# Kernel optimization log

Hardware: AMD Instinct MI355X
Metric: run time of the kernel (lower is better)

## Reference

```python
import jax, jax.numpy as jnp
import numpy as np
from jax import lax

B, C, H, W = 2, 64, 48, 64
RU, RV = 3, 3
U, V = 2 * RU + 1, 2 * RV + 1
D = U * V  # 49 displacements


def setup_inputs() -> dict:
    key = jax.random.key(0)
    ks = jax.random.split(key, 12)
    p = lambda k, shape, s: jax.random.normal(k, shape, jnp.float32) * s
    feat1 = p(ks[0], (B, C, H, W), 1.0)
    feat2 = p(ks[1], (B, C, H, W), 1.0)
    gy, gx = jnp.meshgrid(jnp.arange(H, dtype=jnp.float32), jnp.arange(W, dtype=jnp.float32), indexing='ij')
    base = jnp.broadcast_to(jnp.stack([gx, gy])[None], (B, 2, H, W))  # channel0=x, channel1=y
    coords = base + p(ks[2], (B, 2, H, W), 1.5)
    return {
        'feat1': feat1, 'feat2': feat2, 'coords': coords,
        # MatchingNet (ConvBlock = conv+ReLU, BN folded into conv)
        'w0': p(ks[3], (96, 2 * C, 3, 3), 0.06), 'b0': jnp.zeros((96,), jnp.float32),
        'w1': p(ks[4], (128, 96, 3, 3), 0.05), 'b1': jnp.zeros((128,), jnp.float32),
        'w2': p(ks[5], (128, 128, 3, 3), 0.04), 'b2': jnp.zeros((128,), jnp.float32),
        'w3': p(ks[6], (64, 128, 3, 3), 0.04), 'b3': jnp.zeros((64,), jnp.float32),
        'wd': p(ks[7], (32, 64, 4, 4), 0.05), 'bd': jnp.zeros((32,), jnp.float32),  # deconv k4 s2 p1
        'w5': p(ks[8], (1, 32, 3, 3), 0.1), 'b5': jnp.zeros((1,), jnp.float32),
        # Displacement-aware projection: 1x1 conv over the 49 displacement channels
        'wdap': p(ks[9], (D, D), 0.15),
    }


def _conv(x, w, b, stride=1, pad=1):
    y = lax.conv_general_dilated(x, w, (stride, stride), ((pad, pad), (pad, pad)),
                                 dimension_numbers=('NCHW', 'OIHW', 'NCHW'))
    return y + b[None, :, None, None]


def _warp_with_context(feat2, coords):
    # grid_sample(bilinear, zeros padding, align_corners=True) at coords + every displacement
    b, c, h, w = feat2.shape
    du = jnp.arange(-RU, RU + 1, dtype=feat2.dtype)
    dv = jnp.arange(-RV, RV + 1, dtype=feat2.dtype)
    x = coords[:, 0][:, None, None, :, :] + du[None, None, :, None, None]  # (b,V,U,h,w) via broadcast
    y = coords[:, 1][:, None, None, :, :] + dv[None, :, None, None, None]
    x0 = jnp.floor(x); y0 = jnp.floor(y)
    wx = (x - x0)[:, None]; wy = (y - y0)[:, None]  # (b,1,V,U,h,w)
    x0i = x0.astype(jnp.int32); y0i = y0.astype(jnp.int32)
    feat_flat = feat2.reshape(b, c, h * w)

    def gather(xi, yi):
        valid = (xi >= 0) & (xi < w) & (yi >= 0) & (yi < h)
        idx = jnp.clip(yi, 0, h - 1) * w + jnp.clip(xi, 0, w - 1)
        v = jax.vmap(lambda f, i: f[:, i])(feat_flat, idx.reshape(b, -1))  # (b,c,P)
        v = v.reshape(b, c, V, U, h, w)
        return v * valid[:, None].astype(feat2.dtype)

    v00 = gather(x0i, y0i)
    v01 = gather(x0i + 1, y0i)
    v10 = gather(x0i, y0i + 1)
    v11 = gather(x0i + 1, y0i + 1)
    out = v00 * (1 - wx) * (1 - wy) + v01 * wx * (1 - wy) + v10 * (1 - wx) * wy + v11 * wx * wy
    return out.transpose(0, 2, 3, 1, 4, 5)  # (b, V, U, c, h, w)


def reference(feat1, feat2, coords, w0, b0, w1, b1, w2, b2, w3, b3, wd, bd, w5, b5, wdap):
    b, c, h, w = feat1.shape
    f2 = _warp_with_context(feat2, coords)
    f1 = jnp.broadcast_to(feat1[:, None, None], (b, V, U, c, h, w))
    feat = jnp.concatenate([f1, f2], axis=3).reshape(b * V * U, 2 * c, h, w)
    # MatchingNet
    x = jnp.maximum(_conv(feat, w0, b0), 0)
    x = jnp.maximum(_conv(x, w1, b1, stride=2), 0)
    x = jnp.maximum(_conv(x, w2, b2), 0)
    x = jnp.maximum(_conv(x, w3, b3), 0)
    x = lax.conv_general_dilated(x, wd, (1, 1), ((2, 2), (2, 2)), lhs_dilation=(2, 2),
                                 dimension_numbers=('NCHW', 'OIHW', 'NCHW')) + bd[None, :, None, None]
    x = jnp.maximum(x, 0)
    cost = _conv(x, w5, b5).reshape(b, V, U, h, w)
    # DAP: 1x1 conv across the D displacement channels, no bias
    cost = jnp.einsum('ed,bdhw->behw', wdap, cost.reshape(b, D, h, w)).reshape(b, V, U, h, w)
    prob = jax.nn.softmax(cost.reshape(b, D, h, w), axis=1).reshape(b, V, U, h, w)
    du = jnp.arange(-RU, RU + 1, dtype=feat1.dtype)
    dv = jnp.arange(-RV, RV + 1, dtype=feat1.dtype)
    dx = jnp.sum(prob * du[None, None, :, None, None], axis=(1, 2))
    dy = jnp.sum(prob * dv[None, :, None, None, None], axis=(1, 2))
    return coords + jnp.stack([dx, dy], axis=1)
```

## Files before the change

kernel.cpp:

```cpp
#include <hip/hip_runtime.h>
#include <hip/hip_bf16.h>

using bf16 = __hip_bfloat16;
typedef __attribute__((ext_vector_type(8))) __bf16 bf16x8;
typedef __attribute__((ext_vector_type(4))) float f32x4;

static __device__ __forceinline__ bf16 f2b(float v) { return __float2bfloat16(v); }
static __device__ __forceinline__ float us2f(unsigned short u) {
    return __uint_as_float(((unsigned)u) << 16);
}


__global__ void sentinel_k(float* __restrict__ out, int nel, float val) {
    int i = blockIdx.x * 256 + threadIdx.x;
    if (i < nel) out[i] = val;
}

__global__ void pack_all(const float* __restrict__ w0, const float* __restrict__ w1,
                         const float* __restrict__ w2, const float* __restrict__ w3,
                         const float* __restrict__ wd, bf16* __restrict__ wsw0,
                         bf16* __restrict__ wsw0a, bf16* __restrict__ wsw1,
                         bf16* __restrict__ wsw2, bf16* __restrict__ wsw3,
                         bf16* __restrict__ wswd) {
    int i = blockIdx.x * 256 + threadIdx.x;
    if (i < 110592) {
        int icbase = (i < 55296) ? 64 : 0;
        bf16* dst = (i < 55296) ? wsw0 : wsw0a;
        int o = (i < 55296) ? i : i - 55296;
        int j = o & 7, lane = (o >> 3) & 63;
        int m = lane & 15, q = lane >> 4;
        int cc = (o >> 9) & 1;
        int fragid = o >> 10;
        int t = fragid / 6, ocf = fragid % 6;
        int oc = ocf * 16 + m, ic = cc * 32 + q * 8 + j;
        dst[o] = f2b(w0[((size_t)oc * 128 + icbase + ic) * 9 + t]);
    } else if (i < 307200) {
        int o = i - 110592;
        int j = o & 7, lane = (o >> 3) & 63;
        int m = lane & 15, q = lane >> 4;
        int cc = (o >> 9) % 12;
        int fragid = (o >> 9) / 12;
        int t2 = fragid / 8, ocf = fragid % 8;
        int oc = ocf * 16 + m;
        int pc = cc * 32 + q * 8 + j;
        int dy = (t2 < 2) ? -1 : 0;
        int dx = (t2 & 1) ? 0 : -1;
        int p = pc / 96, ic = pc % 96;
        int py = p >> 1, px = p & 1;
        int ky = (dy == -1) ? (py == 1 ? 0 : -1) : (py == 0 ? 1 : 2);
        int kx = (dx == -1) ? (px == 1 ? 0 : -1) : (px == 0 ? 1 : 2);
        float v = (ky >= 0 && kx >= 0) ? w1[((size_t)oc * 96 + ic) * 9 + ky * 3 + kx] : 0.f;
        wsw1[o] = f2b(v);
    } else if (i < 454656) {
        int o = i - 307200;
        int j = o & 7, lane = (o >> 3) & 63;
        int m = lane & 15, q = lane >> 4;
        int cc = (o >> 9) % 4;
        int fragid = (o >> 9) / 4;
        int t = fragid / 8, ocf = fragid % 8;
        int oc = ocf * 16 + m, ic = cc * 32 + q * 8 + j;
        wsw2[o] = f2b(w2[((size_t)oc * 128 + ic) * 9 + t]);
    } else if (i < 528384) {
        int o = i - 454656;
        int j = o & 7, lane = (o >> 3) & 63;
        int m = lane & 15, q = lane >> 4;
        int cc = (o >> 9) % 4;
        int fragid = (o >> 9) / 4;
        int t = fragid / 4, ocf = fragid % 4;
        int oc = ocf * 16 + m, ic = cc * 32 + q * 8 + j;
        wsw3[o] = f2b(w3[((size_t)oc * 128 + ic) * 9 + t]);
    } else if (i < 561152) {
        int o = i - 528384;
        int j = o & 7, lane = (o >> 3) & 63;
        int m = lane & 15, q = lane >> 4;
        int cc = (o >> 9) & 1;
        int ocf = (o >> 10) & 1;
        int t2 = (o >> 11) & 3;
        int c = o >> 13;
        int oc = ocf * 16 + m, ic = cc * 32 + q * 8 + j;
        int qy = c >> 1, qx = c & 1;
        int dy = qy - 1 + (t2 >> 1), dx = qx - 1 + (t2 & 1);
        int ky = (qy == 0) ? (dy == -1 ? 0 : 2) : (dy == 0 ? 1 : 3);
        int kx = (qx == 0) ? (dx == -1 ? 0 : 2) : (dx == 0 ? 1 : 3);
        wswd[o] = f2b(wd[((size_t)oc * 64 + ic) * 16 + ky * 4 + kx]);
    }
}

__global__ void to_nhwc2(const float* __restrict__ feat1, const float* __restrict__ feat2,
                         bf16* __restrict__ f1n, bf16* __restrict__ f2n) {
    int i = blockIdx.x * 256 + threadIdx.x;
    const float* src = (i < 393216) ? feat1 : feat2;
    bf16* dst = (i < 393216) ? f1n : f2n;
    int o = (i < 393216) ? i : i - 393216;
    if (o >= 393216) return;
    int c = o & 63;
    int p = (o >> 6) % 3072;
    int b = o / (3072 * 64);
    dst[o] = f2b(src[((size_t)b * 64 + c) * 3072 + p]);
}

__global__ __launch_bounds__(256) void warp_kernel(const bf16* __restrict__ f2n,
                                                   const float* __restrict__ coords,
                                                   bf16* __restrict__ f2w, int bd0, int cnt) {
    int idx = blockIdx.x * 256 + threadIdx.x;
    if (idx >= cnt * 3072 * 8) return;
    int g = idx & 7;
    int pix = idx >> 3;
    int p = pix % 3072;
    int z = pix / 3072;
    int bd = bd0 + z;
    int b = bd / 49, d = bd % 49;
    float du = (float)(d % 7 - 3), dv = (float)(d / 7 - 3);
    float cx = coords[(size_t)(b * 2 + 0) * 3072 + p] + du;
    float cy = coords[(size_t)(b * 2 + 1) * 3072 + p] + dv;
    float x0f = floorf(cx), y0f = floorf(cy);
    float wx = cx - x0f, wy = cy - y0f;
    int x0 = (int)x0f, y0 = (int)y0f;
    int x1 = x0 + 1, y1 = y0 + 1;
    bool vx0 = (x0 >= 0) && (x0 < 64), vx1 = (x1 >= 0) && (x1 < 64);
    bool vy0 = (y0 >= 0) && (y0 < 48), vy1 = (y1 >= 0) && (y1 < 48);
    int xc0 = min(max(x0, 0), 63), xc1 = min(max(x1, 0), 63);
    int yc0 = min(max(y0, 0), 47), yc1 = min(max(y1, 0), 47);
    float w00 = (vx0 && vy0) ? (1.f - wx) * (1.f - wy) : 0.f;
    float w01 = (vx1 && vy0) ? wx * (1.f - wy) : 0.f;
    float w10 = (vx0 && vy1) ? (1.f - wx) * wy : 0.f;
    float w11 = (vx1 && vy1) ? wx * wy : 0.f;
    const unsigned short* f2 = (const unsigned short*)f2n + (size_t)b * 3072 * 64 + g * 8;
    ushort4 a0 = *(const ushort4*)(f2 + (size_t)(yc0 * 64 + xc0) * 64);
    ushort4 a1 = *(const ushort4*)(f2 + (size_t)(yc0 * 64 + xc0) * 64 + 4);
    ushort4 b0v = *(const ushort4*)(f2 + (size_t)(yc0 * 64 + xc1) * 64);
    ushort4 b1v = *(const ushort4*)(f2 + (size_t)(yc0 * 64 + xc1) * 64 + 4);
    ushort4 c0 = *(const ushort4*)(f2 + (size_t)(yc1 * 64 + xc0) * 64);
    ushort4 c1 = *(const ushort4*)(f2 + (size_t)(yc1 * 64 + xc0) * 64 + 4);
    ushort4 d0 = *(const ushort4*)(f2 + (size_t)(yc1 * 64 + xc1) * 64);
    ushort4 d1 = *(const ushort4*)(f2 + (size_t)(yc1 * 64 + xc1) * 64 + 4);
    unsigned short ua[8] = {a0.x, a0.y, a0.z, a0.w, a1.x, a1.y, a1.z, a1.w};
    unsigned short ub[8] = {b0v.x, b0v.y, b0v.z, b0v.w, b1v.x, b1v.y, b1v.z, b1v.w};
    unsigned short uc[8] = {c0.x, c0.y, c0.z, c0.w, c1.x, c1.y, c1.z, c1.w};
    unsigned short ud[8] = {d0.x, d0.y, d0.z, d0.w, d1.x, d1.y, d1.z, d1.w};
    unsigned short ro[8];
#pragma unroll
    for (int e = 0; e < 8; ++e) {
        float v = w00 * us2f(ua[e]) + w01 * us2f(ub[e]) + w10 * us2f(uc[e]) + w11 * us2f(ud[e]);
        bf16 r = f2b(v);
        ro[e] = *(unsigned short*)&r;
    }
    unsigned short* outp = (unsigned short*)f2w + ((size_t)z * 3072 + p) * 64 + g * 8;
    *(ushort4*)outp = (ushort4){ro[0], ro[1], ro[2], ro[3]};
    *(ushort4*)(outp + 4) = (ushort4){ro[4], ro[5], ro[6], ro[7]};
}

template <int IC, int OCTOT, int OC_BLK, int H, int W, int MROWS, int NTAPS, int DXW,
          int DYLO, int DXLO, int BMODE, int OMODE>
__global__ __launch_bounds__(512, 4) void conv_ldz(const bf16* __restrict__ in_,
                                                   const bf16* __restrict__ wsw_,
                                                   const float* __restrict__ bias,
                                                   const bf16* __restrict__ base_,
                                                   bf16* __restrict__ out, int bd0, int cnt) {
    constexpr int NCH = IC / 32;
    constexpr int NfT = OC_BLK / 32;
    constexpr int TPXH = MROWS * W / 2;
    constexpr int MF = TPXH / 16;
    constexpr int NDY = NTAPS / DXW;
    constexpr int ROWS_IN = MROWS + NDY - 1;
    constexpr int COLS_IN = W + DXW - 1;
    constexpr int NOCF = OCTOT / 16;
    constexpr int PITCH = 40;
    constexpr int SZA = ROWS_IN * COLS_IN * PITCH;
    constexpr int OUTSH = MROWS * W * OC_BLK;
    constexpr int SMEM = (2 * SZA > OUTSH) ? 2 * SZA : OUTSH;
    __shared__ __align__(16) unsigned short s_mem[SMEM];

    const unsigned short* in = (const unsigned short*)in_;
    const unsigned short* wsw = (const unsigned short*)wsw_;
    const unsigned short* baseh = (const unsigned short*)base_;
    const int tid = threadIdx.x;
    const int wave = tid >> 6, lane = tid & 63;
    const int m = lane & 15, q = lane >> 4;
    const int wz = wave >> 2, wy = (wave >> 1) & 1, wx = wave & 1;
    const int bx = blockIdx.x, by = blockIdx.y;
    const int z0 = blockIdx.z * 2;
    const int zw = z0 + wz;
    const bool zok = zw < cnt;
    const int foff = m * PITCH + q * 8;
    const int ocbase = by * OC_BLK;

    f32x4 acc[MF][NfT];
#pragma unroll
    for (int a = 0; a < MF; ++a)
#pragma unroll
        for (int nf = 0; nf < NfT; ++nf) acc[a][nf] = (f32x4){0.f, 0.f, 0.f, 0.f};

    for (int cc = 0; cc < NCH; ++cc) {
        constexpr int SZE = ROWS_IN * COLS_IN * 4;
        for (int i = tid; i < 2 * SZE; i += 512) {
            int zz = i / SZE;
            int r2 = i % SZE;
            int e = r2 & 3;
            int pix = r2 >> 2;
            int cI = pix % COLS_IN;
            int rr = pix / COLS_IN;
            int gy = bx * MROWS + rr + DYLO;
            int gx = cI + DXLO;
            uint4 v = {0u, 0u, 0u, 0u};
            if ((z0 + zz) < cnt && gy >= 0 && gy < H && gx >= 0 && gx < W)
                v = *(const uint4*)(in +
                                    ((size_t)((z0 + zz) * H + gy) * W + gx) * IC + cc * 32 + e * 8);
            *(uint4*)(&s_mem[zz * SZA + pix * PITCH + e * 8]) = v;
        }
        __syncthreads();
        if (zok) {
            bf16x8 bcur[NfT], bnxt[NfT];
#pragma unroll
            for (int nf = 0; nf < NfT; ++nf) {
                const int fragoc = (ocbase >> 4) + wx * NfT + nf;
                bcur[nf] = *(const bf16x8*)(wsw + (((size_t)0 * NOCF + fragoc) * NCH + cc) * 512 +
                                            lane * 8);
            }
#pragma unroll
            for (int t = 0; t < NTAPS; ++t) {
                if (t + 1 < NTAPS) {
#pragma unroll
                    for (int nf = 0; nf < NfT; ++nf) {
                        const int fragoc = (ocbase >> 4) + wx * NfT + nf;
                        bnxt[nf] = *(const bf16x8*)(wsw +
                                                    (((size_t)(t + 1) * NOCF + fragoc) * NCH + cc) *
                                                        512 +
                                                    lane * 8);
                    }
                }
                bf16x8 af[MF];
#pragma unroll
                for (int mf = 0; mf < MF; ++mf) {
                    const int pxb = wy * TPXH + mf * 16;
                    const int yl = pxb / W, xb = pxb % W;
                    const unsigned short* pa =
                        &s_mem[wz * SZA + ((yl + t / DXW) * COLS_IN + xb + t % DXW) * PITCH] + foff;
                    af[mf] = *(const bf16x8*)pa;
                }
#pragma unroll
                for (int mf = 0; mf < MF; ++mf)
#pragma unroll
                    for (int nf = 0; nf < NfT; ++nf)
                        acc[mf][nf] = __builtin_amdgcn_mfma_f32_16x16x32_bf16(af[mf], bcur[nf],
                                                                              acc[mf][nf], 0, 0, 0);
                if (t + 1 < NTAPS) {
#pragma unroll
                    for (int nf = 0; nf < NfT; ++nf) bcur[nf] = bnxt[nf];
                }
            }
        }
        __syncthreads();
    }

    const int bimg = (bd0 + zw) / 49;
    float bb[NfT];
    if constexpr (BMODE == 0) {
#pragma unroll
        for (int nf = 0; nf < NfT; ++nf) bb[nf] = bias[ocbase + wx * (OC_BLK / 2) + nf * 16 + m];
    }
    for (int zz = 0; zz < 2; ++zz) {
        if (wz == zz && zok) {
#pragma unroll
            for (int mf = 0; mf < MF; ++mf) {
                const int pxb = wy * TPXH + mf * 16;
#pragma unroll
                for (int r = 0; r < 4; ++r) {
                    const int px = pxb + q * 4 + r;
                    const int yl = px / W, xl = px % W;
                    const int gy = bx * MROWS + yl;
#pragma unroll
                    for (int nf = 0; nf < NfT; ++nf) {
                        const int oc = wx * (OC_BLK / 2) + nf * 16 + m;
                        float v = acc[mf][nf][r];
                        if constexpr (BMODE == 1)
                            v += us2f(baseh[(((size_t)bimg * 48 + gy) * 64 + xl) * 96 + ocbase + oc]);
                        else
                            v += bb[nf];
                        if constexpr (OMODE != 4) v = fmaxf(v, 0.f);
                        bf16 bv = f2b(v);
                        s_mem[px * OC_BLK + oc] = *(unsigned short*)&bv;
                    }
                }
            }
        }
        __syncthreads();
        const int z = z0 + zz;
        if (z < cnt) {
            constexpr int TOT16 = MROWS * W * OC_BLK / 8;
            for (int g = tid; g < TOT16; g += 512) {
                const int o = g * 8;
                if constexpr (OMODE == 1) {
                    const int xx = o / 384;
                    const int rr = o % 384;
                    const int pp = rr / 96;
                    const int oco = rr % 96;
                    const int px = (pp >> 1) * 64 + 2 * xx + (pp & 1);
                    uint4 vv = *(const uint4*)&s_mem[px * 96 + oco];
                    *(uint4*)((unsigned short*)out + (((size_t)z * 24 + bx) * 32 + xx) * 384 + rr) =
                        vv;
                } else {
                    uint4 vv = *(const uint4*)&s_mem[o];
                    const int px = o / OC_BLK;
                    const int oco = o % OC_BLK;
                    const int gy = bx * MROWS + px / W;
                    const int xl = px % W;
                    if constexpr (OMODE == 4)
                        *(uint4*)((unsigned short*)out +
                                  (((size_t)z * H + gy) * W + xl) * OCTOT + ocbase + oco) = vv;
                    else
                        *(uint4*)((unsigned short*)out +
                                  (((size_t)z * H + gy) * W + xl) * OCTOT + ocbase + oco) = vv;
                }
            }
        }
        __syncthreads();
    }
}

__global__ __launch_bounds__(512, 4) void deconv_k4(const bf16* __restrict__ in_,
                                                    const bf16* __restrict__ wswd_,
                                                    const float* __restrict__ bias,
                                                    bf16* __restrict__ out, int cnt) {
    constexpr int PITCH = 40;
    constexpr int SZA = 6 * 34 * PITCH;
    __shared__ __align__(16) unsigned short s_mem[16384];

    const unsigned short* in = (const unsigned short*)in_;
    const unsigned short* wsw = (const unsigned short*)wswd_;
    const int tid = threadIdx.x;
    const int wave = tid >> 6, lane = tid & 63;
    const int m = lane & 15, q = lane >> 4;
    const int wz = wave >> 2, cls = wave & 3;
    const int qy = cls >> 1, qx = cls & 1;
    const int bx = blockIdx.x;
    const int z0 = blockIdx.z * 2;
    const int zw = z0 + wz;
    const bool zok = zw < cnt;
    const int foff = m * PITCH + q * 8;

    f32x4 acc[8][2];
#pragma unroll
    for (int a = 0; a < 8; ++a) {
        acc[a][0] = (f32x4){0.f, 0.f, 0.f, 0.f};
        acc[a][1] = (f32x4){0.f, 0.f, 0.f, 0.f};
    }

    for (int cc = 0; cc < 2; ++cc) {
        constexpr int SZE = 6 * 34 * 4;
        for (int i = tid; i < 2 * SZE; i += 512) {
            int zz = i / SZE;
            int r2 = i % SZE;
            int e = r2 & 3;
            int pix = r2 >> 2;
            int cI = pix % 34;
            int rr = pix / 34;
            int gy = bx * 4 + rr - 1;
            int gx = cI - 1;
            uint4 v = {0u, 0u, 0u, 0u};
            if ((z0 + zz) < cnt && gy >= 0 && gy < 24 && gx >= 0 && gx < 32)
                v = *(const uint4*)(in + ((size_t)((z0 + zz) * 24 + gy) * 32 + gx) * 64 + cc * 32 +
                                    e * 8);
            *(uint4*)(&s_mem[zz * SZA + pix * PITCH + e * 8]) = v;
        }
        __syncthreads();
        if (zok) {
            bf16x8 bcur[2], bnxt[2];
#pragma unroll
            for (int nf = 0; nf < 2; ++nf)
                bcur[nf] = *(const bf16x8*)(wsw + cls * 8192 + 0 * 2048 + nf * 1024 + cc * 512 +
                                            lane * 8);
#pragma unroll
            for (int t = 0; t < 4; ++t) {
                if (t + 1 < 4) {
#pragma unroll
                    for (int nf = 0; nf < 2; ++nf)
                        bnxt[nf] = *(const bf16x8*)(wsw + cls * 8192 + (t + 1) * 2048 + nf * 1024 +
                                                    cc * 512 + lane * 8);
                }
                const int dy = qy - 1 + (t >> 1);
                const int dx = qx - 1 + (t & 1);
                bf16x8 af[8];
#pragma unroll
                for (int mf = 0; mf < 8; ++mf) {
                    const int yl = mf >> 1, xb = (mf & 1) * 16;
                    const unsigned short* pa =
                        &s_mem[wz * SZA + ((yl + dy + 1) * 34 + xb + dx + 1) * PITCH] + foff;
                    af[mf] = *(const bf16x8*)pa;
                }
#pragma unroll
                for (int mf = 0; mf < 8; ++mf)
#pragma unroll
                    for (int nf = 0; nf < 2; ++nf)
                        acc[mf][nf] = __builtin_amdgcn_mfma_f32_16x16x32_bf16(af[mf], bcur[nf],
                                                                              acc[mf][nf], 0, 0, 0);
                if (t + 1 < 4) {
                    bcur[0] = bnxt[0];
                    bcur[1] = bnxt[1];
                }
            }
        }
        __syncthreads();
    }

    const float bb0 = bias[m], bb1 = bias[16 + m];
    for (int zz = 0; zz < 2; ++zz) {
        if (wz == zz && zok) {
#pragma unroll
            for (int mf = 0; mf < 8; ++mf) {
#pragma unroll
                for (int r = 0; r < 4; ++r) {
                    const int px = mf * 16 + q * 4 + r;
                    const int yl = px >> 5, xl = px & 31;
                    const int opx = (2 * yl + qy) * 64 + 2 * xl + qx;
                    float v0 = fmaxf(acc[mf][0][r] + bb0, 0.f);
                    float v1 = fmaxf(acc[mf][1][r] + bb1, 0.f);
                    bf16 b0 = f2b(v0), b1 = f2b(v1);
                    s_mem[opx * 32 + m] = *(unsigned short*)&b0;
                    s_mem[opx * 32 + 16 + m] = *(unsigned short*)&b1;
                }
            }
        }
        __syncthreads();
        const int z = z0 + zz;
        if (z < cnt) {
            for (int g = tid; g < 2048; g += 512) {
                const int o = g * 8;
                *(uint4*)((unsigned short*)out + ((size_t)z * 3072 + bx * 512) * 32 + o) =
                    *(const uint4*)&s_mem[o];
            }
        }
        __syncthreads();
    }
}

__global__ __launch_bounds__(256) void conv5_k(const bf16* __restrict__ in_,
                                               const float* __restrict__ w5,
                                               const float* __restrict__ b5,
                                               float* __restrict__ cost, int bd0, int cnt) {
    __shared__ float s_w5[9][32];
    const int tid = threadIdx.x;
    for (int i = tid; i < 288; i += 256) {
        int ic = i % 32, t = i / 32;
        s_w5[t][ic] = w5[ic * 9 + t];
    }
    __syncthreads();
    int idx = blockIdx.x * 256 + tid;
    if (idx >= cnt * 3072) return;
    int p = idx % 3072, z = idx / 3072;
    int y = p >> 6, x = p & 63;
    const unsigned short* in = (const unsigned short*)in_;
    float acc = b5[0];
#pragma unroll
    for (int ky = 0; ky < 3; ++ky) {
        int gy = y + ky - 1;
        if (gy < 0 || gy >= 48) continue;
#pragma unroll
        for (int kx = 0; kx < 3; ++kx) {
            int gx = x + kx - 1;
            if (gx < 0 || gx >= 64) continue;
            const ushort4* src = (const ushort4*)(in + ((size_t)(z * 48 + gy) * 64 + gx) * 32);
            const float* wr = s_w5[ky * 3 + kx];
#pragma unroll
            for (int e = 0; e < 8; ++e) {
                ushort4 u = src[e];
                acc = fmaf(us2f(u.x), wr[e * 4 + 0], acc);
                acc = fmaf(us2f(u.y), wr[e * 4 + 1], acc);
                acc = fmaf(us2f(u.z), wr[e * 4 + 2], acc);
                acc = fmaf(us2f(u.w), wr[e * 4 + 3], acc);
            }
        }
    }
    cost[(size_t)(bd0 + z) * 3072 + p] = acc;
}

__global__ __launch_bounds__(256) void dap_flow(const float* __restrict__ cost,
                                                const float* __restrict__ wdap,
                                                const float* __restrict__ coords,
                                                float* __restrict__ outp) {
    __shared__ float s_w[49 * 49];
    int tid = threadIdx.x;
    for (int i = tid; i < 2401; i += 256) s_w[i] = wdap[i];
    __syncthreads();
    int idx = blockIdx.x * 256 + tid;
    if (idx >= 2 * 3072) return;
    int p = idx % 3072, b = idx / 3072;
    float c[49];
#pragma unroll
    for (int d = 0; d < 49; ++d) c[d] = cost[((size_t)(b * 49 + d)) * 3072 + p];
    float mx = -1e30f;
    for (int e = 0; e < 49; ++e) {
        float s = 0.f;
#pragma unroll
        for (int d = 0; d < 49; ++d) s = fmaf(s_w[e * 49 + d], c[d], s);
        mx = fmaxf(mx, s);
    }
    float sum = 0.f, sx = 0.f, sy = 0.f;
    for (int e = 0; e < 49; ++e) {
        float s = 0.f;
#pragma unroll
        for (int d = 0; d < 49; ++d) s = fmaf(s_w[e * 49 + d], c[d], s);
        float pr = __expf(s - mx);
        sum += pr;
        sx += pr * (float)(e % 7 - 3);
        sy += pr * (float)(e / 7 - 3);
    }
    float inv = 1.f / sum;
    outp[(size_t)(b * 2 + 0) * 3072 + p] = coords[(size_t)(b * 2 + 0) * 3072 + p] + sx * inv;
    outp[(size_t)(b * 2 + 1) * 3072 + p] = coords[(size_t)(b * 2 + 1) * 3072 + p] + sy * inv;
}

extern "C" void kernel_launch(void* const* d_in, const int* in_sizes, int n_in,
                              void* d_out, int out_size, void* d_ws, size_t ws_size,
                              hipStream_t stream) {
    (void)in_sizes; (void)n_in;
    const float* feat1 = (const float*)d_in[0];
    const float* feat2 = (const float*)d_in[1];
    const float* coords = (const float*)d_in[2];
    const float* w0 = (const float*)d_in[3];
    const float* b0 = (const float*)d_in[4];
    const float* w1 = (const float*)d_in[5];
    const float* b1 = (const float*)d_in[6];
    const float* w2 = (const float*)d_in[7];
    const float* b2 = (const float*)d_in[8];
    const float* w3 = (const float*)d_in[9];
    const float* b3 = (const float*)d_in[10];
    const float* wd = (const float*)d_in[11];
    const float* bdc = (const float*)d_in[12];
    const float* w5 = (const float*)d_in[13];
    const float* b5 = (const float*)d_in[14];
    const float* wdap = (const float*)d_in[15];
    float* outp = (float*)d_out;

    char* ws = (char*)d_ws;
    bf16* wsw0 = (bf16*)(ws + 0);
    bf16* wsw0a = (bf16*)(ws + 110592);
    bf16* wsw1 = (bf16*)(ws + 221184);
    bf16* wsw2 = (bf16*)(ws + 614400);
    bf16* wsw3 = (bf16*)(ws + 909312);
    bf16* wswd = (bf16*)(ws + 1056768);
    bf16* f1n = (bf16*)(ws + 1122304);
    bf16* part0 = (bf16*)(ws + 1908736);
    float* cost = (float*)(ws + 3088384);
    bf16* f2n = (bf16*)(ws + 4292608);
    const size_t fixed_end = 5079040;

    const int cand[7] = {98, 49, 25, 14, 7, 2, 1};
    int nb = 0;
    for (int i = 0; i < 7; ++i) {
        if (fixed_end + (size_t)983040 * cand[i] <= ws_size) { nb = cand[i]; break; }
    }
    if (nb == 0) {
        float val = 10000.f + (float)(ws_size >> 20);
        sentinel_k<<<dim3((out_size + 255) / 256), 256, 0, stream>>>(outp, out_size, val);
        return;
    }
    char* regA = ws + fixed_end;
    char* regB = regA + (size_t)393216 * nb;
    bf16* f2w = (bf16*)regA;
    bf16* x1 = (bf16*)regA;
    bf16* x3 = (bf16*)regA;
    bf16* x0p = (bf16*)regB;
    bf16* x2 = (bf16*)regB;
    bf16* xd = (bf16*)regB;

    pack_all<<<dim3(2192), 256, 0, stream>>>(w0, w1, w2, w3, wd, wsw0, wsw0a, wsw1, wsw2, wsw3,
                                             wswd);
    to_nhwc2<<<dim3(3072), 256, 0, stream>>>(feat1, feat2, f1n, f2n);
    conv_ldz<64, 96, 96, 48, 64, 2, 9, 3, -1, -1, 0, 4>
        <<<dim3(24, 1, 1), 512, 0, stream>>>(f1n, wsw0a, b0, nullptr, part0, 0, 2);

    for (int s = 0; s < 98; s += nb) {
        int cnt = (98 - s < nb) ? (98 - s) : nb;
        int zp = (cnt + 1) / 2;
        warp_kernel<<<dim3(cnt * 96), 256, 0, stream>>>(f2n, coords, f2w, s, cnt);
        conv_ldz<64, 96, 96, 48, 64, 2, 9, 3, -1, -1, 1, 1>
            <<<dim3(24, 1, zp), 512, 0, stream>>>(f2w, wsw0, nullptr, part0, x0p, s, cnt);
        conv_ldz<384, 128, 64, 24, 32, 4, 4, 2, -1, -1, 0, 0>
            <<<dim3(6, 2, zp), 512, 0, stream>>>(x0p, wsw1, b1, nullptr, x1, s, cnt);
        conv_ldz<128, 128, 64, 24, 32, 4, 9, 3, -1, -1, 0, 0>
            <<<dim3(6, 2, zp), 512, 0, stream>>>(x1, wsw2, b2, nullptr, x2, s, cnt);
        conv_ldz<128, 64, 32, 24, 32, 4, 9, 3, -1, -1, 0, 0>
            <<<dim3(6, 2, zp), 512, 0, stream>>>(x2, wsw3, b3, nullptr, x3, s, cnt);
        deconv_k4<<<dim3(6, 1, zp), 512, 0, stream>>>(x3, wswd, bdc, xd, cnt);
        conv5_k<<<dim3(cnt * 12), 256, 0, stream>>>(xd, w5, b5, cost, s, cnt);
    }

    dap_flow<<<dim3(24), 256, 0, stream>>>(cost, wdap, coords, outp);
}
```

Baseline: 389.8 us.

## Split conv blocks to one image per 256-thread block with 4-wave pixel split

Conv and deconv kernels previously processed two images per 512-thread block, with waves split over image, pixel half and OC half. They now process one image per 256-thread block, with the four waves splitting pixels and each wave covering all OC fragments. This halves shared memory per block and drops the cnt guards and per-image store loop. Each wave holds more accumulators, so register pressure goes up, and weight fragments are loaded per wave across the full OC block. The conv3 launch also changes from OC_BLK 32 with two OC blocks to a single OC block of 64.

```diff
diff --git a/kernel.cpp b/kernel.cpp
--- a/kernel.cpp
+++ b/kernel.cpp
@@ -152,15 +152,15 @@
 
 template <int IC, int OCTOT, int OC_BLK, int H, int W, int MROWS, int NTAPS, int DXW,
           int DYLO, int DXLO, int BMODE, int OMODE>
-__global__ __launch_bounds__(512, 4) void conv_ldz(const bf16* __restrict__ in_,
+__global__ __launch_bounds__(256, 4) void conv_px4(const bf16* __restrict__ in_,
                                                    const bf16* __restrict__ wsw_,
                                                    const float* __restrict__ bias,
                                                    const bf16* __restrict__ base_,
-                                                   bf16* __restrict__ out, int bd0, int cnt) {
+                                                   bf16* __restrict__ out, int bd0) {
     constexpr int NCH = IC / 32;
-    constexpr int NfT = OC_BLK / 32;
-    constexpr int TPXH = MROWS * W / 2;
-    constexpr int MF = TPXH / 16;
+    constexpr int NfT = OC_BLK / 16;
+    constexpr int TPXQ = MROWS * W / 4;
+    constexpr int MF = TPXQ / 16;
     constexpr int NDY = NTAPS / DXW;
     constexpr int ROWS_IN = MROWS + NDY - 1;
     constexpr int COLS_IN = W + DXW - 1;
@@ -168,20 +168,16 @@
     constexpr int PITCH = 40;
     constexpr int SZA = ROWS_IN * COLS_IN * PITCH;
     constexpr int OUTSH = MROWS * W * OC_BLK;
-    constexpr int SMEM = (2 * SZA > OUTSH) ? 2 * SZA : OUTSH;
+    constexpr int SMEM = (SZA > OUTSH) ? SZA : OUTSH;
     __shared__ __align__(16) unsigned short s_mem[SMEM];
 
     const unsigned short* in = (const unsigned short*)in_;
     const unsigned short* wsw = (const unsigned short*)wsw_;
     const unsigned short* baseh = (const unsigned short*)base_;
     const int tid = threadIdx.x;
-    const int wave = tid >> 6, lane = tid & 63;
+    const int wp = tid >> 6, lane = tid & 63;
     const int m = lane & 15, q = lane >> 4;
-    const int wz = wave >> 2, wy = (wave >> 1) & 1, wx = wave & 1;
-    const int bx = blockIdx.x, by = blockIdx.y;
-    const int z0 = blockIdx.z * 2;
-    const int zw = z0 + wz;
-    const bool zok = zw < cnt;
+    const int bx = blockIdx.x, by = blockIdx.y, z = blockIdx.z;
     const int foff = m * PITCH + q * 8;
     const int ocbase = by * OC_BLK;
 
@@ -193,27 +189,24 @@
 
     for (int cc = 0; cc < NCH; ++cc) {
         constexpr int SZE = ROWS_IN * COLS_IN * 4;
-        for (int i = tid; i < 2 * SZE; i += 512) {
-            int zz = i / SZE;
-            int r2 = i % SZE;
-            int e = r2 & 3;
-            int pix = r2 >> 2;
+        for (int i = tid; i < SZE; i += 256) {
+            int e = i & 3;
+            int pix = i >> 2;
             int cI = pix % COLS_IN;
             int rr = pix / COLS_IN;
             int gy = bx * MROWS + rr + DYLO;
             int gx = cI + DXLO;
             uint4 v = {0u, 0u, 0u, 0u};
-            if ((z0 + zz) < cnt && gy >= 0 && gy < H && gx >= 0 && gx < W)
-                v = *(const uint4*)(in +
-                                    ((size_t)((z0 + zz) * H + gy) * W + gx) * IC + cc * 32 + e * 8);
-            *(uint4*)(&s_mem[zz * SZA + pix * PITCH + e * 8]) = v;
+            if (gy >= 0 && gy < H && gx >= 0 && gx < W)
+                v = *(const uint4*)(in + ((size_t)(z * H + gy) * W + gx) * IC + cc * 32 + e * 8);
+            *(uint4*)(&s_mem[pix * PITCH + e * 8]) = v;
         }
         __syncthreads();
-        if (zok) {
+        {
             bf16x8 bcur[NfT], bnxt[NfT];
 #pragma unroll
             for (int nf = 0; nf < NfT; ++nf) {
-                const int fragoc = (ocbase >> 4) + wx * NfT + nf;
+                const int fragoc = (ocbase >> 4) + nf;
                 bcur[nf] = *(const bf16x8*)(wsw + (((size_t)0 * NOCF + fragoc) * NCH + cc) * 512 +
                                             lane * 8);
             }
@@ -222,7 +215,7 @@
                 if (t + 1 < NTAPS) {
 #pragma unroll
                     for (int nf = 0; nf < NfT; ++nf) {
-                        const int fragoc = (ocbase >> 4) + wx * NfT + nf;
+                        const int fragoc = (ocbase >> 4) + nf;
                         bnxt[nf] = *(const bf16x8*)(wsw +
                                                     (((size_t)(t + 1) * NOCF + fragoc) * NCH + cc) *
                                                         512 +
@@ -232,10 +225,10 @@
                 bf16x8 af[MF];
 #pragma unroll
                 for (int mf = 0; mf < MF; ++mf) {
-                    const int pxb = wy * TPXH + mf * 16;
+                    const int pxb = wp * TPXQ + mf * 16;
                     const int yl = pxb / W, xb = pxb % W;
                     const unsigned short* pa =
-                        &s_mem[wz * SZA + ((yl + t / DXW) * COLS_IN + xb + t % DXW) * PITCH] + foff;
+                        &s_mem[((yl + t / DXW) * COLS_IN + xb + t % DXW) * PITCH] + foff;
                     af[mf] = *(const bf16x8*)pa;
                 }
 #pragma unroll
@@ -253,90 +246,73 @@
         __syncthreads();
     }
 
-    const int bimg = (bd0 + zw) / 49;
+    const int bimg = (bd0 + z) / 49;
     float bb[NfT];
     if constexpr (BMODE == 0) {
 #pragma unroll
-        for (int nf = 0; nf < NfT; ++nf) bb[nf] = bias[ocbase + wx * (OC_BLK / 2) + nf * 16 + m];
-    }
-    for (int zz = 0; zz < 2; ++zz) {
-        if (wz == zz && zok) {
-#pragma unroll
-            for (int mf = 0; mf < MF; ++mf) {
-                const int pxb = wy * TPXH + mf * 16;
-#pragma unroll
-                for (int r = 0; r < 4; ++r) {
-                    const int px = pxb + q * 4 + r;
-                    const int yl = px / W, xl = px % W;
-                    const int gy = bx * MROWS + yl;
-#pragma unroll
-                    for (int nf = 0; nf < NfT; ++nf) {
-                        const int oc = wx * (OC_BLK / 2) + nf * 16 + m;
-                        float v = acc[mf][nf][r];
-                        if constexpr (BMODE == 1)
-                            v += us2f(baseh[(((size_t)bimg * 48 + gy) * 64 + xl) * 96 + ocbase + oc]);
-                        else
-                            v += bb[nf];
-                        if constexpr (OMODE != 4) v = fmaxf(v, 0.f);
-                        bf16 bv = f2b(v);
-                        s_mem[px * OC_BLK + oc] = *(unsigned short*)&bv;
-                    }
-                }
+        for (int nf = 0; nf < NfT; ++nf) bb[nf] = bias[ocbase + nf * 16 + m];
+    }
+#pragma unroll
+    for (int mf = 0; mf < MF; ++mf) {
+        const int pxb = wp * TPXQ + mf * 16;
+#pragma unroll
+        for (int r = 0; r < 4; ++r) {
+            const int px = pxb + q * 4 + r;
+            const int yl = px / W, xl = px % W;
+            const int gy = bx * MROWS + yl;
+#pragma unroll
+            for (int nf = 0; nf < NfT; ++nf) {
+                const int oc = nf * 16 + m;
+                float v = acc[mf][nf][r];
+                if constexpr (BMODE == 1)
+                    v += us2f(baseh[(((size_t)bimg * 48 + gy) * 64 + xl) * 96 + ocbase + oc]);
+                else
+                    v += bb[nf];
+                if constexpr (OMODE != 4) v = fmaxf(v, 0.f);
+                bf16 bv = f2b(v);
+                s_mem[px * OC_BLK + oc] = *(unsigned short*)&bv;
             }
         }
-        __syncthreads();
-        const int z = z0 + zz;
-        if (z < cnt) {
-            constexpr int TOT16 = MROWS * W * OC_BLK / 8;
-            for (int g = tid; g < TOT16; g += 512) {
-                const int o = g * 8;
-                if constexpr (OMODE == 1) {
-                    const int xx = o / 384;
-                    const int rr = o % 384;
-                    const int pp = rr / 96;
-                    const int oco = rr % 96;
-                    const int px = (pp >> 1) * 64 + 2 * xx + (pp & 1);
-                    uint4 vv = *(const uint4*)&s_mem[px * 96 + oco];
-                    *(uint4*)((unsigned short*)out + (((size_t)z * 24 + bx) * 32 + xx) * 384 + rr) =
-                        vv;
-                } else {
-                    uint4 vv = *(const uint4*)&s_mem[o];
-                    const int px = o / OC_BLK;
-                    const int oco = o % OC_BLK;
-                    const int gy = bx * MROWS + px / W;
-                    const int xl = px % W;
-                    if constexpr (OMODE == 4)
-                        *(uint4*)((unsigned short*)out +
-                                  (((size_t)z * H + gy) * W + xl) * OCTOT + ocbase + oco) = vv;
-                    else
-                        *(uint4*)((unsigned short*)out +
-                                  (((size_t)z * H + gy) * W + xl) * OCTOT + ocbase + oco) = vv;
-                }
-            }
-        }
-        __syncthreads();
-    }
-}
-
-__global__ __launch_bounds__(512, 4) void deconv_k4(const bf16* __restrict__ in_,
+    }
+    __syncthreads();
+    constexpr int TOT16 = MROWS * W * OC_BLK / 8;
+    for (int g = tid; g < TOT16; g += 256) {
+        const int o = g * 8;
+        if constexpr (OMODE == 1) {
+            const int xx = o / 384;
+            const int rr = o % 384;
+            const int pp = rr / 96;
+            const int oco = rr % 96;
+            const int px = (pp >> 1) * 64 + 2 * xx + (pp & 1);
+            uint4 vv = *(const uint4*)&s_mem[px * 96 + oco];
+            *(uint4*)((unsigned short*)out + (((size_t)z * 24 + bx) * 32 + xx) * 384 + rr) = vv;
+        } else {
+            uint4 vv = *(const uint4*)&s_mem[o];
+            const int px = o / OC_BLK;
+            const int oco = o % OC_BLK;
+            const int gy = bx * MROWS + px / W;
+            const int xl = px % W;
+            *(uint4*)((unsigned short*)out + (((size_t)z * H + gy) * W + xl) * OCTOT + ocbase +
+                      oco) = vv;
+        }
+    }
+}
+
+__global__ __launch_bounds__(256, 4) void deconv_c4(const bf16* __restrict__ in_,
                                                     const bf16* __restrict__ wswd_,
                                                     const float* __restrict__ bias,
-                                                    bf16* __restrict__ out, int cnt) {
+                                                    bf16* __restrict__ out) {
     constexpr int PITCH = 40;
-    constexpr int SZA = 6 * 34 * PITCH;
     __shared__ __align__(16) unsigned short s_mem[16384];
 
     const unsigned short* in = (const unsigned short*)in_;
     const unsigned short* wsw = (const unsigned short*)wswd_;
     const int tid = threadIdx.x;
-    const int wave = tid >> 6, lane = tid & 63;
+    const int cls = tid >> 6, lane = tid & 63;
     const int m = lane & 15, q = lane >> 4;
-    const int wz = wave >> 2, cls = wave & 3;
     const int qy = cls >> 1, qx = cls & 1;
     const int bx = blockIdx.x;
-    const int z0 = blockIdx.z * 2;
-    const int zw = z0 + wz;
-    const bool zok = zw < cnt;
+    const int z = blockIdx.y;
     const int foff = m * PITCH + q * 8;
 
     f32x4 acc[8][2];
@@ -348,28 +324,24 @@
 
     for (int cc = 0; cc < 2; ++cc) {
         constexpr int SZE = 6 * 34 * 4;
-        for (int i = tid; i < 2 * SZE; i += 512) {
-            int zz = i / SZE;
-            int r2 = i % SZE;
-            int e = r2 & 3;
-            int pix = r2 >> 2;
+        for (int i = tid; i < SZE; i += 256) {
+            int e = i & 3;
+            int pix = i >> 2;
             int cI = pix % 34;
             int rr = pix / 34;
             int gy = bx * 4 + rr - 1;
             int gx = cI - 1;
             uint4 v = {0u, 0u, 0u, 0u};
-            if ((z0 + zz) < cnt && gy >= 0 && gy < 24 && gx >= 0 && gx < 32)
-                v = *(const uint4*)(in + ((size_t)((z0 + zz) * 24 + gy) * 32 + gx) * 64 + cc * 32 +
-                                    e * 8);
-            *(uint4*)(&s_mem[zz * SZA + pix * PITCH + e * 8]) = v;
+            if (gy >= 0 && gy < 24 && gx >= 0 && gx < 32)
+                v = *(const uint4*)(in + ((size_t)(z * 24 + gy) * 32 + gx) * 64 + cc * 32 + e * 8);
+            *(uint4*)(&s_mem[pix * PITCH + e * 8]) = v;
         }
         __syncthreads();
-        if (zok) {
+        {
             bf16x8 bcur[2], bnxt[2];
 #pragma unroll
             for (int nf = 0; nf < 2; ++nf)
-                bcur[nf] = *(const bf16x8*)(wsw + cls * 8192 + 0 * 2048 + nf * 1024 + cc * 512 +
-                                            lane * 8);
+                bcur[nf] = *(const bf16x8*)(wsw + cls * 8192 + nf * 1024 + cc * 512 + lane * 8);
 #pragma unroll
             for (int t = 0; t < 4; ++t) {
                 if (t + 1 < 4) {
@@ -385,7 +357,7 @@
                 for (int mf = 0; mf < 8; ++mf) {
                     const int yl = mf >> 1, xb = (mf & 1) * 16;
                     const unsigned short* pa =
-                        &s_mem[wz * SZA + ((yl + dy + 1) * 34 + xb + dx + 1) * PITCH] + foff;
+                        &s_mem[((yl + dy + 1) * 34 + xb + dx + 1) * PITCH] + foff;
                     af[mf] = *(const bf16x8*)pa;
                 }
 #pragma unroll
@@ -404,33 +376,25 @@
     }
 
     const float bb0 = bias[m], bb1 = bias[16 + m];
-    for (int zz = 0; zz < 2; ++zz) {
-        if (wz == zz && zok) {
-#pragma unroll
-            for (int mf = 0; mf < 8; ++mf) {
-#pragma unroll
-                for (int r = 0; r < 4; ++r) {
-                    const int px = mf * 16 + q * 4 + r;
-                    const int yl = px >> 5, xl = px & 31;
-                    const int opx = (2 * yl + qy) * 64 + 2 * xl + qx;
-                    float v0 = fmaxf(acc[mf][0][r] + bb0, 0.f);
-                    float v1 = fmaxf(acc[mf][1][r] + bb1, 0.f);
-                    bf16 b0 = f2b(v0), b1 = f2b(v1);
-                    s_mem[opx * 32 + m] = *(unsigned short*)&b0;
-                    s_mem[opx * 32 + 16 + m] = *(unsigned short*)&b1;
-                }
-            }
-        }
-        __syncthreads();
-        const int z = z0 + zz;
-        if (z < cnt) {
-            for (int g = tid; g < 2048; g += 512) {
-                const int o = g * 8;
-                *(uint4*)((unsigned short*)out + ((size_t)z * 3072 + bx * 512) * 32 + o) =
-                    *(const uint4*)&s_mem[o];
-            }
-        }
-        __syncthreads();
+#pragma unroll
+    for (int mf = 0; mf < 8; ++mf) {
+#pragma unroll
+        for (int r = 0; r < 4; ++r) {
+            const int px = mf * 16 + q * 4 + r;
+            const int yl = px >> 5, xl = px & 31;
+            const int opx = (2 * yl + qy) * 64 + 2 * xl + qx;
+            float v0 = fmaxf(acc[mf][0][r] + bb0, 0.f);
+            float v1 = fmaxf(acc[mf][1][r] + bb1, 0.f);
+            bf16 b0 = f2b(v0), b1 = f2b(v1);
+            s_mem[opx * 32 + m] = *(unsigned short*)&b0;
+            s_mem[opx * 32 + 16 + m] = *(unsigned short*)&b1;
+        }
+    }
+    __syncthreads();
+    for (int g = tid; g < 2048; g += 256) {
+        const int o = g * 8;
+        *(uint4*)((unsigned short*)out + ((size_t)z * 3072 + bx * 512) * 32 + o) =
+            *(const uint4*)&s_mem[o];
     }
 }
 
@@ -567,22 +531,21 @@
     pack_all<<<dim3(2192), 256, 0, stream>>>(w0, w1, w2, w3, wd, wsw0, wsw0a, wsw1, wsw2, wsw3,
                                              wswd);
     to_nhwc2<<<dim3(3072), 256, 0, stream>>>(feat1, feat2, f1n, f2n);
-    conv_ldz<64, 96, 96, 48, 64, 2, 9, 3, -1, -1, 0, 4>
-        <<<dim3(24, 1, 1), 512, 0, stream>>>(f1n, wsw0a, b0, nullptr, part0, 0, 2);
+    conv_px4<64, 96, 96, 48, 64, 2, 9, 3, -1, -1, 0, 4>
+        <<<dim3(24, 1, 2), 256, 0, stream>>>(f1n, wsw0a, b0, nullptr, part0, 0);
 
     for (int s = 0; s < 98; s += nb) {
         int cnt = (98 - s < nb) ? (98 - s) : nb;
-        int zp = (cnt + 1) / 2;
         warp_kernel<<<dim3(cnt * 96), 256, 0, stream>>>(f2n, coords, f2w, s, cnt);
-        conv_ldz<64, 96, 96, 48, 64, 2, 9, 3, -1, -1, 1, 1>
-            <<<dim3(24, 1, zp), 512, 0, stream>>>(f2w, wsw0, nullptr, part0, x0p, s, cnt);
-        conv_ldz<384, 128, 64, 24, 32, 4, 4, 2, -1, -1, 0, 0>
-            <<<dim3(6, 2, zp), 512, 0, stream>>>(x0p, wsw1, b1, nullptr, x1, s, cnt);
-        conv_ldz<128, 128, 64, 24, 32, 4, 9, 3, -1, -1, 0, 0>
-            <<<dim3(6, 2, zp), 512, 0, stream>>>(x1, wsw2, b2, nullptr, x2, s, cnt);
-        conv_ldz<128, 64, 32, 24, 32, 4, 9, 3, -1, -1, 0, 0>
-            <<<dim3(6, 2, zp), 512, 0, stream>>>(x2, wsw3, b3, nullptr, x3, s, cnt);
-        deconv_k4<<<dim3(6, 1, zp), 512, 0, stream>>>(x3, wswd, bdc, xd, cnt);
+        conv_px4<64, 96, 96, 48, 64, 2, 9, 3, -1, -1, 1, 1>
+            <<<dim3(24, 1, cnt), 256, 0, stream>>>(f2w, wsw0, nullptr, part0, x0p, s);
+        conv_px4<384, 128, 64, 24, 32, 4, 4, 2, -1, -1, 0, 0>
+            <<<dim3(6, 2, cnt), 256, 0, stream>>>(x0p, wsw1, b1, nullptr, x1, s);
+        conv_px4<128, 128, 64, 24, 32, 4, 9, 3, -1, -1, 0, 0>
+            <<<dim3(6, 2, cnt), 256, 0, stream>>>(x1, wsw2, b2, nullptr, x2, s);
+        conv_px4<128, 64, 64, 24, 32, 4, 9, 3, -1, -1, 0, 0>
+            <<<dim3(6, 1, cnt), 256, 0, stream>>>(x2, wsw3, b3, nullptr, x3, s);
+        deconv_c4<<<dim3(6, cnt), 256, 0, stream>>>(x3, wswd, bdc, xd);
         conv5_k<<<dim3(cnt * 12), 256, 0, stream>>>(xd, w5, b5, cost, s, cnt);
     }
 
```

Result: faster. 369.7 us (-5.2%).
